# Optimization experiments

Measured on AMD Instinct MI355X. Metric: run time of the kernel, lower is better.

The kernel has to match this reference:

```python
import jax, jax.numpy as jnp
import numpy as np

B, D, R = 16384, 4096, 64       # batch tokens, embed_dim, low_rank_dimension
N_PART = 8                       # number of subspace partitions
P = R // N_PART                  # partition size = 8
N_SEL = 4                        # partitions selected per example


def setup_inputs() -> dict:
    key = jax.random.key(0)
    k1, k2, k3, k4 = jax.random.split(key, 4)
    base = jax.random.normal(k1, (B, D), dtype=jnp.float32)
    source = jax.random.normal(k2, (B, D), dtype=jnp.float32)
    # orthogonal low-rank rotation (torch.nn.utils.parametrizations.orthogonal)
    W, _ = jnp.linalg.qr(jax.random.normal(k3, (D, R), dtype=jnp.float32))  # [D, R], orthonormal cols
    subspaces = jax.random.randint(k4, (B, N_SEL), 0, N_PART)               # partition ids per example
    return {"base": base, "source": source, "W": W, "subspaces": subspaces}


def reference(base, source, W, subspaces):
    # rotate into low-rank space: [B, R]
    rotated_base = base @ W
    rotated_source = source @ W
    diff = rotated_source - rotated_base

    # per-example selected rotated-space indices (contiguous partitions of size P)
    # idx[b] = concat over selected partitions of [p*P, p*P+P)
    idx = (subspaces[:, :, None] * P + jnp.arange(P)).reshape(B, N_SEL * P)  # [B, N_SEL*P]

    # Selecting columns of diff and matching rows of W.T, then matmul, is
    # equivalent to masking unselected rotated dims to zero and doing one GEMM.
    mask = jnp.zeros((B, R), dtype=diff.dtype).at[jnp.arange(B)[:, None], idx].set(1.0)
    output = base + (diff * mask) @ W.T  # [B, D]
    return output.astype(base.dtype)
```

## Files before the change

### kernel.cpp

```cpp
#include <hip/hip_runtime.h>


#define D_DIM 4096
#define R_DIM 64
#define BM1   16
#define BM2   32

typedef short bf16vec8 __attribute__((ext_vector_type(8)));
typedef float f32x4v  __attribute__((ext_vector_type(4)));

__device__ __forceinline__ unsigned int f2bf_u(float f) {
  unsigned int u = __builtin_bit_cast(unsigned int, f);
  return (u + 0x7fffu + ((u >> 16) & 1u)) >> 16;
}
__device__ __forceinline__ unsigned int pack2bf(float a, float b) {
  return f2bf_u(a) | (f2bf_u(b) << 16);
}
__device__ __forceinline__ void async_ld16(const void* g, void* l) {
  __builtin_amdgcn_global_load_lds(
      (const __attribute__((address_space(1))) void*)g,
      (__attribute__((address_space(3))) void*)l, 16, 0, 0);
}

__global__ __launch_bounds__(256)
void lrri_prep(const float* __restrict__ W, unsigned short* __restrict__ Wt,
               unsigned short* __restrict__ Wb) {
  const int idx = blockIdx.x * blockDim.x + threadIdx.x;
  const int k = idx >> 4;
  const int j = (idx & 15) * 4;
  float4 w = *(const float4*)(W + (size_t)k * R_DIM + j);
  ushort4 p;
  p.x = (unsigned short)f2bf_u(w.x);
  p.y = (unsigned short)f2bf_u(w.y);
  p.z = (unsigned short)f2bf_u(w.z);
  p.w = (unsigned short)f2bf_u(w.w);
  *(ushort4*)(Wb + (size_t)k * R_DIM + j) = p;
  Wt[(size_t)(j + 0) * D_DIM + k] = p.x;
  Wt[(size_t)(j + 1) * D_DIM + k] = p.y;
  Wt[(size_t)(j + 2) * D_DIM + k] = p.z;
  Wt[(size_t)(j + 3) * D_DIM + k] = p.w;
}

__global__ __launch_bounds__(256, 3)
void k1_rotdiff(const float* __restrict__ base, const float* __restrict__ srcp,
                const int* __restrict__ subs,
                const unsigned short* __restrict__ Wt_bf,
                unsigned short* __restrict__ rm_g)
{
  __shared__ __align__(16) float part[4][64 * 17];
  const int tid  = threadIdx.x;
  const int wave = tid >> 6;
  const int lane = tid & 63;
  const int l4   = lane & 15;
  const int g    = lane >> 4;
  const long rowbase = (long)blockIdx.x * BM1;
  const long rowA    = (rowbase + l4) * (long)D_DIM;
  const int  kq0     = wave * 1024;
  const int  off1    = (blockIdx.x * 5) & 15;

  f32x4v acc[4];
  #pragma unroll
  for (int t = 0; t < 4; ++t) acc[t] = (f32x4v){0.f, 0.f, 0.f, 0.f};

  auto loadd = [&](int c, float4 (&vb)[4], float4 (&vs)[4]) {
    const int ch = (c + off1) & 15;
    const long colf = kq0 + ch * 64;
    #pragma unroll
    for (int q = 0; q < 4; ++q) {
      const long off = rowA + colf + (q >> 1) * 32 + g * 8 + (q & 1) * 4;
      vb[q] = *(const float4*)(base + off);
      vs[q] = *(const float4*)(srcp + off);
    }
  };

  auto comp = [&](int c, const float4 (&vb)[4], const float4 (&vs)[4]) {
    const int ch = (c + off1) & 15;
    const long colf = kq0 + ch * 64;
    uint4 df[2];
    #pragma unroll
    for (int s = 0; s < 2; ++s) {
      float d0 = vs[s*2].x - vb[s*2].x, d1 = vs[s*2].y - vb[s*2].y;
      float d2 = vs[s*2].z - vb[s*2].z, d3 = vs[s*2].w - vb[s*2].w;
      float d4 = vs[s*2+1].x - vb[s*2+1].x, d5 = vs[s*2+1].y - vb[s*2+1].y;
      float d6 = vs[s*2+1].z - vb[s*2+1].z, d7 = vs[s*2+1].w - vb[s*2+1].w;
      df[s].x = pack2bf(d0, d1);
      df[s].y = pack2bf(d2, d3);
      df[s].z = pack2bf(d4, d5);
      df[s].w = pack2bf(d6, d7);
    }
    #pragma unroll
    for (int t = 0; t < 4; ++t) {
      #pragma unroll
      for (int s = 0; s < 2; ++s) {
        uint4 wf = *(const uint4*)(Wt_bf + (size_t)(t * 16 + l4) * D_DIM +
                                   colf + s * 32 + g * 8);
        acc[t] = __builtin_amdgcn_mfma_f32_16x16x32_bf16(
            __builtin_bit_cast(bf16vec8, wf),
            __builtin_bit_cast(bf16vec8, df[s]),
            acc[t], 0, 0, 0);
      }
    }
  };

  float4 b0[4], s0[4], b1[4], s1[4];
  loadd(0, b0, s0);
  #pragma unroll 1
  for (int cc = 0; cc < 14; cc += 2) {
    loadd(cc + 1, b1, s1);
    comp(cc, b0, s0);
    loadd(cc + 2, b0, s0);
    comp(cc + 1, b1, s1);
  }
  loadd(15, b1, s1);
  comp(14, b0, s0);
  comp(15, b1, s1);

  #pragma unroll
  for (int t = 0; t < 4; ++t)
    #pragma unroll
    for (int i = 0; i < 4; ++i)
      part[wave][(t * 16 + g * 4 + i) * 17 + l4] = acc[t][i];
  __syncthreads();

  {
    const int row = tid >> 4, jg = tid & 15;
    int4 sb = *(const int4*)(subs + (rowbase + row) * 4);
    unsigned mbits = (1u << sb.x) | (1u << sb.y) | (1u << sb.z) | (1u << sb.w);
    unsigned short v[4];
    #pragma unroll
    for (int jj = 0; jj < 4; ++jj) {
      const int j = jg * 4 + jj;
      float sum = part[0][j * 17 + row] + part[1][j * 17 + row] +
                  part[2][j * 17 + row] + part[3][j * 17 + row];
      v[jj] = ((mbits >> (j >> 3)) & 1u) ? (unsigned short)f2bf_u(sum)
                                         : (unsigned short)0;
    }
    uint2 pk;
    pk.x = (unsigned)v[0] | ((unsigned)v[1] << 16);
    pk.y = (unsigned)v[2] | ((unsigned)v[3] << 16);
    *(uint2*)(rm_g + (rowbase + row) * 64 + jg * 4) = pk;
  }
}

__global__ __launch_bounds__(256, 4)
void k2_apply(const float* __restrict__ base,
              const unsigned short* __restrict__ rm_g,
              const unsigned short* __restrict__ Wb_bf,
              float* __restrict__ out)
{
  __shared__ __align__(16) unsigned char smem[36864];
  const int tid  = threadIdx.x;
  const int wave = tid >> 6;
  const int lane = tid & 63;
  const int l4   = lane & 15;
  const int g    = lane >> 4;
  const long rowbase = (long)blockIdx.x * BM2;
  const int off2 = (blockIdx.x * 5) & 15;

  uint4 a2[2][2];
  #pragma unroll
  for (int m = 0; m < 2; ++m)
    #pragma unroll
    for (int s = 0; s < 2; ++s)
      a2[m][s] = *(const uint4*)(rm_g + (rowbase + m * 16 + l4) * 64 +
                                 s * 32 + g * 8);

  float* cbuf = (float*)(smem + wave * 9216);
  #pragma unroll 1
  for (int grp = 0; grp < 16; ++grp) {
    const int ga = (grp + off2) & 15;
    const int cbase = wave * 1024 + ga * 64;
    float4 bb[8];
    #pragma unroll
    for (int v2 = 0; v2 < 8; ++v2) {
      const int r = g + v2 * 4;
      bb[v2] = *(const float4*)(base + (rowbase + r) * D_DIM + cbase + l4 * 4);
    }
    f32x4v a[2][4];
    #pragma unroll
    for (int m = 0; m < 2; ++m)
      #pragma unroll
      for (int t = 0; t < 4; ++t) a[m][t] = (f32x4v){0.f, 0.f, 0.f, 0.f};
    #pragma unroll
    for (int t = 0; t < 4; ++t) {
      #pragma unroll
      for (int s = 0; s < 2; ++s) {
        uint4 bfrag = *(const uint4*)(Wb_bf +
            (size_t)(cbase + t * 16 + l4) * R_DIM + s * 32 + g * 8);
        #pragma unroll
        for (int m = 0; m < 2; ++m)
          a[m][t] = __builtin_amdgcn_mfma_f32_16x16x32_bf16(
              __builtin_bit_cast(bf16vec8, a2[m][s]),
              __builtin_bit_cast(bf16vec8, bfrag), a[m][t], 0, 0, 0);
      }
    }
    #pragma unroll
    for (int m = 0; m < 2; ++m)
      #pragma unroll
      for (int t = 0; t < 4; ++t)
        #pragma unroll
        for (int i = 0; i < 4; ++i)
          cbuf[(m * 16 + g * 4 + i) * 72 + t * 16 + l4] = a[m][t][i];
    __syncthreads();
    #pragma unroll
    for (int v2 = 0; v2 < 8; ++v2) {
      const int r = g + v2 * 4;
      f32x4v cv = *(const f32x4v*)(cbuf + r * 72 + l4 * 4);
      float4 o;
      o.x = cv[0] + bb[v2].x;
      o.y = cv[1] + bb[v2].y;
      o.z = cv[2] + bb[v2].z;
      o.w = cv[3] + bb[v2].w;
      *(float4*)(out + (rowbase + r) * D_DIM + cbase + l4 * 4) = o;
    }
    __syncthreads();
  }
}

__global__ __launch_bounds__(256, 2)
void lrri_fused_nows(const float* __restrict__ base, const float* __restrict__ srcp,
                     const float* __restrict__ W, const int* __restrict__ subs,
                     float* __restrict__ out)
{
  __shared__ __align__(16) unsigned char smem[70144];
  const int tid  = threadIdx.x;
  const int wave = tid >> 6;
  const int lane = tid & 63;
  const int l4   = lane & 15;
  const int g    = lane >> 4;
  const int rh   = wave >> 1;
  const int kh   = wave & 1;
  const long rowbase = (long)blockIdx.x * BM2;
  const long rowg    = rowbase + rh * 16;
  unsigned char* wbuf = smem + wave * 16384;
  const int off1 = (blockIdx.x * 7) & 63;
  const int off2 = (blockIdx.x * 5) & 15;

  f32x4v acc[4];
  #pragma unroll
  for (int t = 0; t < 4; ++t) acc[t] = (f32x4v){0.f, 0.f, 0.f, 0.f};

  #pragma unroll 1
  for (int c = 0; c < 64; ++c) {
    const int ch = (c + off1) & 63;
    unsigned char* buf = wbuf + (c & 1) * 8192;
    const long colf = kh * 2048 + ch * 32;
    #pragma unroll
    for (int q = 0; q < 2; ++q) {
      const int r = q * 8 + (lane >> 3);
      const unsigned b = ((unsigned)((lane & 7) * 16)) ^ ((unsigned)(r & 7) << 4);
      const long goff = (rowg + r) * (long)D_DIM + colf + (b >> 2);
      async_ld16(base + goff, buf + q * 1024);
      async_ld16(srcp + goff, buf + 2048 + q * 1024);
    }
    asm volatile("s_waitcnt vmcnt(0)" ::: "memory");
    __builtin_amdgcn_sched_barrier(0);
    const unsigned sw = (unsigned)((l4 & 7) << 4);
    const unsigned c0 = ((unsigned)(g * 32)) ^ sw;
    const unsigned c1 = ((unsigned)(g * 32 + 16)) ^ sw;
    float4 fb0 = *(const float4*)(buf + l4 * 128 + c0);
    float4 fb1 = *(const float4*)(buf + l4 * 128 + c1);
    float4 fs0 = *(const float4*)(buf + 2048 + l4 * 128 + c0);
    float4 fs1 = *(const float4*)(buf + 2048 + l4 * 128 + c1);
    uint4 af;
    af.x = pack2bf(fs0.x - fb0.x, fs0.y - fb0.y);
    af.y = pack2bf(fs0.z - fb0.z, fs0.w - fb0.w);
    af.z = pack2bf(fs1.x - fb1.x, fs1.y - fb1.y);
    af.w = pack2bf(fs1.z - fb1.z, fs1.w - fb1.w);
    #pragma unroll
    for (int t = 0; t < 4; ++t) {
      unsigned int pq[4];
      #pragma unroll
      for (int e2 = 0; e2 < 4; ++e2) {
        float wa = W[(size_t)(colf + g * 8 + e2 * 2    ) * R_DIM + t * 16 + l4];
        float wb = W[(size_t)(colf + g * 8 + e2 * 2 + 1) * R_DIM + t * 16 + l4];
        pq[e2] = pack2bf(wa, wb);
      }
      uint4 wf; wf.x = pq[0]; wf.y = pq[1]; wf.z = pq[2]; wf.w = pq[3];
      acc[t] = __builtin_amdgcn_mfma_f32_16x16x32_bf16(
          __builtin_bit_cast(bf16vec8, af),
          __builtin_bit_cast(bf16vec8, wf), acc[t], 0, 0, 0);
    }
  }

  {
    float* part = (float*)wbuf;
    #pragma unroll
    for (int t = 0; t < 4; ++t)
      #pragma unroll
      for (int i = 0; i < 4; ++i)
        part[(g * 4 + i) * 72 + t * 16 + l4] = acc[t][i];
  }
  __syncthreads();

  {
    const int row = tid >> 3, jg = tid & 7;
    const int lr  = row & 15;
    const float* pa = (const float*)(smem + ((row >> 4) * 2 + 0) * 16384);
    const float* pb = (const float*)(smem + ((row >> 4) * 2 + 1) * 16384);
    int4 sb = *(const int4*)(subs + (rowbase + row) * 4);
    unsigned mbits = (1u << sb.x) | (1u << sb.y) | (1u << sb.z) | (1u << sb.w);
    unsigned short v[8];
    #pragma unroll
    for (int jj = 0; jj < 8; ++jj) {
      const int j = jg * 8 + jj;
      float sum = pa[lr * 72 + j] + pb[lr * 72 + j];
      v[jj] = ((mbits >> (j >> 3)) & 1u) ? (unsigned short)f2bf_u(sum)
                                         : (unsigned short)0;
    }
    uint4 pk;
    pk.x = (unsigned)v[0] | ((unsigned)v[1] << 16);
    pk.y = (unsigned)v[2] | ((unsigned)v[3] << 16);
    pk.z = (unsigned)v[4] | ((unsigned)v[5] << 16);
    pk.w = (unsigned)v[6] | ((unsigned)v[7] << 16);
    *(uint4*)(smem + 65536 + row * 144 + jg * 16) = pk;
  }
  __syncthreads();

  uint4 a2[2][2];
  #pragma unroll
  for (int m = 0; m < 2; ++m)
    #pragma unroll
    for (int s = 0; s < 2; ++s)
      a2[m][s] = *(const uint4*)(smem + 65536 + (m * 16 + l4) * 144 +
                                 s * 64 + g * 16);
  float* cbuf = (float*)wbuf;
  #pragma unroll 1
  for (int grp = 0; grp < 16; ++grp) {
    const int ga = (grp + off2) & 15;
    const int cbase = wave * 1024 + ga * 64;
    float4 bb[8];
    #pragma unroll
    for (int v2 = 0; v2 < 8; ++v2) {
      const int r = g + v2 * 4;
      bb[v2] = *(const float4*)(base + (rowbase + r) * D_DIM + cbase + l4 * 4);
    }
    f32x4v a[2][4];
    #pragma unroll
    for (int m = 0; m < 2; ++m)
      #pragma unroll
      for (int t = 0; t < 4; ++t) a[m][t] = (f32x4v){0.f, 0.f, 0.f, 0.f};
    #pragma unroll
    for (int t = 0; t < 4; ++t) {
      #pragma unroll
      for (int s = 0; s < 2; ++s) {
        const float* wp = W + (size_t)(cbase + t * 16 + l4) * R_DIM + s * 32 + g * 8;
        float4 wa = *(const float4*)(wp);
        float4 wb2 = *(const float4*)(wp + 4);
        uint4 bfrag;
        bfrag.x = pack2bf(wa.x, wa.y); bfrag.y = pack2bf(wa.z, wa.w);
        bfrag.z = pack2bf(wb2.x, wb2.y); bfrag.w = pack2bf(wb2.z, wb2.w);
        #pragma unroll
        for (int m = 0; m < 2; ++m)
          a[m][t] = __builtin_amdgcn_mfma_f32_16x16x32_bf16(
              __builtin_bit_cast(bf16vec8, a2[m][s]),
              __builtin_bit_cast(bf16vec8, bfrag), a[m][t], 0, 0, 0);
      }
    }
    #pragma unroll
    for (int m = 0; m < 2; ++m)
      #pragma unroll
      for (int t = 0; t < 4; ++t)
        #pragma unroll
        for (int i = 0; i < 4; ++i)
          cbuf[(m * 16 + g * 4 + i) * 72 + t * 16 + l4] = a[m][t][i];
    #pragma unroll
    for (int v2 = 0; v2 < 8; ++v2) {
      const int r = g + v2 * 4;
      f32x4v cv = *(const f32x4v*)(cbuf + r * 72 + l4 * 4);
      float4 o;
      o.x = cv[0] + bb[v2].x;
      o.y = cv[1] + bb[v2].y;
      o.z = cv[2] + bb[v2].z;
      o.w = cv[3] + bb[v2].w;
      *(float4*)(out + (rowbase + r) * D_DIM + cbase + l4 * 4) = o;
    }
  }
}

extern "C" void kernel_launch(void* const* d_in, const int* in_sizes, int n_in,
                              void* d_out, int out_size, void* d_ws, size_t ws_size,
                              hipStream_t stream) {
  const float* base = (const float*)d_in[0];
  const float* srcp = (const float*)d_in[1];
  const float* W    = (const float*)d_in[2];
  const int*   subs = (const int*)d_in[3];
  float* out = (float*)d_out;

  const size_t wconv = (size_t)2 * R_DIM * D_DIM * sizeof(unsigned short);
  const size_t rmsz  = (size_t)16384 * R_DIM * sizeof(unsigned short);
  if (d_ws && ws_size >= wconv + rmsz) {
    unsigned short* Wt = (unsigned short*)d_ws;
    unsigned short* Wb = Wt + (size_t)R_DIM * D_DIM;
    unsigned short* rm = Wb + (size_t)R_DIM * D_DIM;
    lrri_prep<<<256, 256, 0, stream>>>(W, Wt, Wb);
    k1_rotdiff<<<16384 / BM1, 256, 0, stream>>>(base, srcp, subs, Wt, rm);
    k2_apply<<<16384 / BM2, 256, 0, stream>>>(base, rm, Wb, out);
  } else {
    lrri_fused_nows<<<16384 / BM2, 256, 0, stream>>>(base, srcp, W, subs, out);
  }
}
```

Before: 263.3 us.

## Split k1 K-reduction across eight waves with 512-thread blocks

Doubles the k1_rotdiff block to 512 threads so eight waves each handle a 512-column slice of the K dimension instead of four waves with 1024 columns. The chunk loop is shortened to 8 and fully unrolled, and the cross-wave reduction now sums eight partials, with each thread writing two outputs. This aims to put more waves in flight per row tile to hide the latency of the streamed base/source loads. It doubles the LDS partial buffer, lengthens the reduction, and the launch bound of 8 blocks per SM constrains register use.

```diff
diff --git a/kernel.cpp b/kernel.cpp
--- a/kernel.cpp
+++ b/kernel.cpp
@@ -41,13 +41,13 @@
   Wt[(size_t)(j + 3) * D_DIM + k] = p.w;
 }
 
-__global__ __launch_bounds__(256, 3)
+__global__ __launch_bounds__(512, 8)
 void k1_rotdiff(const float* __restrict__ base, const float* __restrict__ srcp,
                 const int* __restrict__ subs,
                 const unsigned short* __restrict__ Wt_bf,
                 unsigned short* __restrict__ rm_g)
 {
-  __shared__ __align__(16) float part[4][64 * 17];
+  __shared__ __align__(16) float part[8][64 * 17];
   const int tid  = threadIdx.x;
   const int wave = tid >> 6;
   const int lane = tid & 63;
@@ -55,15 +55,15 @@
   const int g    = lane >> 4;
   const long rowbase = (long)blockIdx.x * BM1;
   const long rowA    = (rowbase + l4) * (long)D_DIM;
-  const int  kq0     = wave * 1024;
-  const int  off1    = (blockIdx.x * 5) & 15;
+  const int  kq0     = wave * 512;
+  const int  off1    = (blockIdx.x * 5) & 7;
 
   f32x4v acc[4];
   #pragma unroll
   for (int t = 0; t < 4; ++t) acc[t] = (f32x4v){0.f, 0.f, 0.f, 0.f};
 
   auto loadd = [&](int c, float4 (&vb)[4], float4 (&vs)[4]) {
-    const int ch = (c + off1) & 15;
+    const int ch = (c + off1) & 7;
     const long colf = kq0 + ch * 64;
     #pragma unroll
     for (int q = 0; q < 4; ++q) {
@@ -74,7 +74,7 @@
   };
 
   auto comp = [&](int c, const float4 (&vb)[4], const float4 (&vs)[4]) {
-    const int ch = (c + off1) & 15;
+    const int ch = (c + off1) & 7;
     const long colf = kq0 + ch * 64;
     uint4 df[2];
     #pragma unroll
@@ -104,16 +104,14 @@
 
   float4 b0[4], s0[4], b1[4], s1[4];
   loadd(0, b0, s0);
-  #pragma unroll 1
-  for (int cc = 0; cc < 14; cc += 2) {
-    loadd(cc + 1, b1, s1);
-    comp(cc, b0, s0);
-    loadd(cc + 2, b0, s0);
-    comp(cc + 1, b1, s1);
-  }
-  loadd(15, b1, s1);
-  comp(14, b0, s0);
-  comp(15, b1, s1);
+  loadd(1, b1, s1); comp(0, b0, s0);
+  loadd(2, b0, s0); comp(1, b1, s1);
+  loadd(3, b1, s1); comp(2, b0, s0);
+  loadd(4, b0, s0); comp(3, b1, s1);
+  loadd(5, b1, s1); comp(4, b0, s0);
+  loadd(6, b0, s0); comp(5, b1, s1);
+  loadd(7, b1, s1); comp(6, b0, s0);
+  comp(7, b1, s1);
 
   #pragma unroll
   for (int t = 0; t < 4; ++t)
@@ -123,22 +121,22 @@
   __syncthreads();
 
   {
-    const int row = tid >> 4, jg = tid & 15;
+    const int row = tid >> 5, jg = tid & 31;
+    const int j0 = jg * 2;
     int4 sb = *(const int4*)(subs + (rowbase + row) * 4);
     unsigned mbits = (1u << sb.x) | (1u << sb.y) | (1u << sb.z) | (1u << sb.w);
-    unsigned short v[4];
-    #pragma unroll
-    for (int jj = 0; jj < 4; ++jj) {
-      const int j = jg * 4 + jj;
-      float sum = part[0][j * 17 + row] + part[1][j * 17 + row] +
-                  part[2][j * 17 + row] + part[3][j * 17 + row];
+    unsigned short v[2];
+    #pragma unroll
+    for (int jj = 0; jj < 2; ++jj) {
+      const int j = j0 + jj;
+      float sum = 0.f;
+      #pragma unroll
+      for (int w = 0; w < 8; ++w) sum += part[w][j * 17 + row];
       v[jj] = ((mbits >> (j >> 3)) & 1u) ? (unsigned short)f2bf_u(sum)
                                          : (unsigned short)0;
     }
-    uint2 pk;
-    pk.x = (unsigned)v[0] | ((unsigned)v[1] << 16);
-    pk.y = (unsigned)v[2] | ((unsigned)v[3] << 16);
-    *(uint2*)(rm_g + (rowbase + row) * 64 + jg * 4) = pk;
+    *(unsigned int*)(rm_g + (rowbase + row) * 64 + j0) =
+        (unsigned)v[0] | ((unsigned)v[1] << 16);
   }
 }
 
@@ -394,7 +392,7 @@
     unsigned short* Wb = Wt + (size_t)R_DIM * D_DIM;
     unsigned short* rm = Wb + (size_t)R_DIM * D_DIM;
     lrri_prep<<<256, 256, 0, stream>>>(W, Wt, Wb);
-    k1_rotdiff<<<16384 / BM1, 256, 0, stream>>>(base, srcp, subs, Wt, rm);
+    k1_rotdiff<<<16384 / BM1, 512, 0, stream>>>(base, srcp, subs, Wt, rm);
     k2_apply<<<16384 / BM2, 256, 0, stream>>>(base, rm, Wb, out);
   } else {
     lrri_fused_nows<<<16384 / BM2, 256, 0, stream>>>(base, srcp, W, subs, out);
```

Result: faster. 256.0 us (-2.8%).
